# Kernel tuning notes

Hardware: AMD Instinct MI355X
Metric: run time of the kernel (lower is better)

Reference implementation:

```python
import jax, jax.numpy as jnp
import numpy as np

NUM_CLASSES = 3
STRIDES = (8, 16, 32)


def _decode(out, stride):
    # out: [B, 5+C, H, W] -> [B, H*W, 5+C] decoded to image coords; also return grid [H*W, 2]
    B, C, H, W = out.shape
    yv, xv = jnp.meshgrid(jnp.arange(H), jnp.arange(W), indexing='ij')
    grid = jnp.stack([xv, yv], -1).reshape(H * W, 2).astype(out.dtype)
    o = out.reshape(B, C, H * W).transpose(0, 2, 1)
    xy = (o[..., :2] + grid[None]) * stride
    wh = jnp.exp(o[..., 2:4]) * stride
    return jnp.concatenate([xy, wh, o[..., 4:]], -1), grid


def _pairwise_iou(gt, pr):
    # gt [G,4], pr [A,4], cxcywh -> iou [G,A]
    tl = jnp.maximum(gt[:, None, :2] - gt[:, None, 2:] / 2, pr[None, :, :2] - pr[None, :, 2:] / 2)
    br = jnp.minimum(gt[:, None, :2] + gt[:, None, 2:] / 2, pr[None, :, :2] + pr[None, :, 2:] / 2)
    en = (tl < br).all(-1).astype(gt.dtype)
    area_i = jnp.prod(br - tl, -1) * en
    area_u = jnp.prod(gt[:, None, 2:], -1) + jnp.prod(pr[None, :, 2:], -1) - area_i
    return area_i / (area_u + 1e-16)


def _iou_loss(pred, target):
    # elementwise IOUloss (loss_type='iou'): 1 - iou^2, shapes [..., 4]
    tl = jnp.maximum(pred[..., :2] - pred[..., 2:] / 2, target[..., :2] - target[..., 2:] / 2)
    br = jnp.minimum(pred[..., :2] + pred[..., 2:] / 2, target[..., :2] + target[..., 2:] / 2)
    en = (tl < br).all(-1).astype(pred.dtype)
    area_i = jnp.prod(br - tl, -1) * en
    area_u = jnp.prod(pred[..., 2:], -1) + jnp.prod(target[..., 2:], -1) - area_i
    iou = area_i / (area_u + 1e-16)
    return 1.0 - iou ** 2


def _bce_logits(x, y):
    # stable BCEWithLogits, reduction='none'
    return jnp.maximum(x, 0) - x * y + jnp.log1p(jnp.exp(-jnp.abs(x)))


def _assign(gt_boxes, gt_cls, box_p, cls_p, obj_p, xs, ys, strides):
    # SimOTA for one image. gt_boxes [G,4], gt_cls [G], box_p [A,4], cls_p [A,C], obj_p [A,1]
    G = gt_boxes.shape[0]
    C = cls_p.shape[-1]
    xc = (xs + 0.5) * strides  # [A] anchor centers in image coords
    yc = (ys + 0.5) * strides
    # anchors inside gt boxes
    gl = gt_boxes[:, 0:1] - gt_boxes[:, 2:3] / 2
    gr = gt_boxes[:, 0:1] + gt_boxes[:, 2:3] / 2
    gt_ = gt_boxes[:, 1:2] - gt_boxes[:, 3:4] / 2
    gb = gt_boxes[:, 1:2] + gt_boxes[:, 3:4] / 2
    in_box = (xc[None] > gl) & (xc[None] < gr) & (yc[None] > gt_) & (yc[None] < gb)  # [G,A]
    # anchors inside center radius 2.5 * stride
    r = 2.5
    in_ctr = ((xc[None] > gt_boxes[:, 0:1] - r * strides[None]) &
              (xc[None] < gt_boxes[:, 0:1] + r * strides[None]) &
              (yc[None] > gt_boxes[:, 1:2] - r * strides[None]) &
              (yc[None] < gt_boxes[:, 1:2] + r * strides[None]))
    cand = in_box.any(0) | in_ctr.any(0)  # [A] candidate anchors (fg_mask)
    in_both = in_box & in_ctr  # [G,A]
    ious = jnp.where(cand[None], _pairwise_iou(gt_boxes, box_p), 0.0)
    iou_cost = -jnp.log(ious + 1e-8)
    p = jnp.sqrt(jax.nn.sigmoid(cls_p) * jax.nn.sigmoid(obj_p))  # [A,C]
    y = jax.nn.one_hot(gt_cls, C, dtype=p.dtype)  # [G,C]
    cls_cost = -(jnp.einsum('gc,ac->ga', y, jnp.log(p + 1e-8)) +
                 jnp.einsum('gc,ac->ga', 1 - y, jnp.log(1 - p + 1e-8)))
    cost = cls_cost + 3.0 * iou_cost + 1e5 * (~in_both).astype(p.dtype)
    cost = jnp.where(cand[None], cost, 1e9)
    # dynamic-k: k_g = clamp(int(sum of top-10 ious), 1)
    topk_ious, _ = jax.lax.top_k(ious, 10)
    dyn_k = jnp.clip(topk_ious.sum(-1).astype(jnp.int32), 1, None)  # [G]
    ranks = jnp.argsort(jnp.argsort(cost, axis=1), axis=1)
    matching = (ranks < dyn_k[:, None]) & cand[None]  # [G,A]
    # resolve anchors matched to multiple gts by min cost
    multi = matching.sum(0) > 1  # [A]
    best = jnp.arange(G)[:, None] == jnp.argmin(cost, axis=0)[None]  # [G,A]
    matching = jnp.where(multi[None], best, matching)
    fg = matching.any(0)  # [A]
    matched_gt = jnp.argmax(matching, axis=0)  # [A]
    pred_iou = (matching.astype(p.dtype) * ious).sum(0)  # [A]
    cls_t = jax.nn.one_hot(gt_cls[matched_gt], C, dtype=p.dtype) * pred_iou[:, None]  # [A,C]
    reg_t = gt_boxes[matched_gt]  # [A,4]
    return fg, cls_t, reg_t


def _forward(p3, p4, p5, mask_inputs, labels, input_images, mask_labels, now_epoch):
    outs, grids, str_list = [], [], []
    for o, s in zip((p3, p4, p5), STRIDES):
        dec, g = _decode(o, float(s))
        outs.append(dec)
        grids.append(g)
        str_list.append(jnp.full((g.shape[0],), float(s), dtype=dec.dtype))
    outputs = jnp.concatenate(outs, 1)  # [B, A, 5+C]
    xs = jnp.concatenate([g[:, 0] for g in grids], 0)  # [A]
    ys = jnp.concatenate([g[:, 1] for g in grids], 0)
    strides = jnp.concatenate(str_list, 0)
    box_p = outputs[..., :4]
    obj_p = outputs[..., 4:5]
    cls_p = outputs[..., 5:]
    gt_boxes = labels[..., :4]
    gt_cls = labels[..., 4].astype(jnp.int32)
    fg, cls_t, reg_t = jax.vmap(_assign, in_axes=(0, 0, 0, 0, 0, None, None, None))(
        gt_boxes, gt_cls, box_p, cls_p, obj_p, xs, ys, strides)
    # assignment is @torch.no_grad() in the original
    fg, cls_t, reg_t = jax.lax.stop_gradient((fg, cls_t, reg_t))
    fgf = fg.astype(outputs.dtype)  # [B,A]
    num_fg = jnp.maximum(fgf.sum(), 1.0)
    loss_iou = (_iou_loss(box_p, reg_t) * fgf).sum()
    loss_obj = _bce_logits(obj_p[..., 0], fgf).sum()
    loss_cls = (_bce_logits(cls_p, cls_t) * fgf[..., None]).sum()
    # segmentation losses: CE (mean NLL over pixels) + Dice
    logp = jax.nn.log_softmax(mask_inputs, axis=1)  # [B,C,H,W]
    ce = -jnp.take_along_axis(logp, mask_labels[:, None].astype(jnp.int32), axis=1).mean()
    sm = jax.nn.softmax(mask_inputs, axis=1).transpose(0, 2, 3, 1)  # [B,H,W,C]
    oh = jax.nn.one_hot(mask_labels, NUM_CLASSES + 1, dtype=sm.dtype)[..., :NUM_CLASSES]
    tp = (oh * sm).sum((0, 1, 2))
    fp = sm.sum((0, 1, 2)) - tp
    fn = oh.sum((0, 1, 2)) - tp
    smooth = 1e-5
    dice = 1.0 - jnp.mean((2 * tp + smooth) / (2 * tp + fn + fp + smooth))  # beta=1
    loss_mask = ce + dice
    loss_sc = jnp.zeros((), outputs.dtype)  # is_sc=False
    reg_w = 5.0
    total = (reg_w * loss_iou + loss_obj + loss_cls + loss_sc) / num_fg + loss_mask
    return jnp.stack([total, reg_w * loss_iou / num_fg, loss_obj / num_fg,
                      loss_cls / num_fg, loss_mask, loss_sc / num_fg])


def setup_inputs() -> dict:
    key = jax.random.key(0)
    ks = jax.random.split(key, 8)
    B, IMG, G = 8, 1024, 20
    C5 = NUM_CLASSES + 5
    p3 = jax.random.normal(ks[0], (B, C5, 128, 128), jnp.float32)
    p4 = jax.random.normal(ks[1], (B, C5, 64, 64), jnp.float32)
    p5 = jax.random.normal(ks[2], (B, C5, 32, 32), jnp.float32)
    mask_inputs = jax.random.normal(ks[3], (B, NUM_CLASSES, IMG, IMG), jnp.float32)
    cxy = jax.random.uniform(ks[4], (B, G, 2), jnp.float32, 64.0, float(IMG - 64))
    wh = jax.random.uniform(ks[5], (B, G, 2), jnp.float32, 16.0, 256.0)
    cls = jax.random.randint(ks[6], (B, G, 1), 0, NUM_CLASSES).astype(jnp.float32)
    labels = jnp.concatenate([cxy, wh, cls], -1)  # [B,G,5] (cx,cy,w,h,class)
    input_images = jax.random.uniform(ks[7], (B, 1, IMG, IMG), jnp.float32)
    mask_labels = jax.random.randint(jax.random.fold_in(key, 9), (B, IMG, IMG), 0, NUM_CLASSES)
    return {"p3": p3, "p4": p4, "p5": p5, "mask_inputs": mask_inputs,
            "labels": labels, "input_images": input_images,
            "mask_labels": mask_labels, "now_epoch": 0}


def reference(p3, p4, p5, mask_inputs, labels, input_images, mask_labels, now_epoch):
    return _forward(p3, p4, p5, mask_inputs, labels, input_images, mask_labels, now_epoch)
```

## Files before the change

### kernel.cpp

```cpp
#include <hip/hip_runtime.h>
#include <cfloat>

constexpr int A_TOT = 21504;
constexpr int NB    = 8;
constexpr int NG    = 20;
constexpr int HW_M  = 1 << 20;
constexpr int SPLIT = 16;
constexpr int CHUNK = A_TOT / SPLIT;
constexpr int MBLK  = 2048;
constexpr int MS1 = 416, MS2 = 416, MS3 = 800, MS4 = 416;
constexpr int MOFF1 = 0, MOFF2 = 416, MOFF3 = 832, MOFF4 = 1632;

constexpr float L2E = 1.44269504088896340736f;
constexpr float LN2 = 0.69314718055994530942f;

constexpr size_t SZ_GA    = (size_t)NB * NG * A_TOT;
constexpr size_t OFF_IOUS = 0;
constexpr size_t OFF_COST = OFF_IOUS + SZ_GA;
constexpr size_t OFF_THRC = OFF_COST + SZ_GA;
constexpr size_t OFF_THRI = OFF_THRC + NB * NG;
constexpr size_t OFF_PM   = OFF_THRI + NB * NG;
constexpr size_t OFF_PK   = OFF_PM + 672 * 4;
constexpr size_t OFF_PV   = OFF_PK + (size_t)MBLK * 10;
constexpr size_t SZ_PART  = (size_t)NB * NG * SPLIT * 10;
constexpr size_t OFF_PC   = OFF_PV + SZ_PART;
constexpr size_t OFF_PI   = OFF_PC + SZ_PART;

__device__ __forceinline__ float hw_exp2(float x) { return __builtin_amdgcn_exp2f(x); }
__device__ __forceinline__ float hw_log2(float x) { return __builtin_amdgcn_logf(x); }
__device__ __forceinline__ float fexp(float x) { return hw_exp2(x * L2E); }
__device__ __forceinline__ float flog(float x) { return hw_log2(x) * LN2; }
__device__ __forceinline__ float frcp(float x) { return __builtin_amdgcn_rcpf(x); }
__device__ __forceinline__ float fsig(float x) { return frcp(1.f + fexp(-x)); }
__device__ __forceinline__ float fbce(float x, float y) {
  float t = hw_exp2(-fabsf(x) * L2E);
  return fmaxf(x, 0.f) - x * y + LN2 * hw_log2(1.f + t);
}
__device__ __forceinline__ void anchor_geom(int a, int& hw, int& lw, float& st) {
  if (a < 16384)      { hw = a;         lw = 7; st = 8.f;  }
  else if (a < 20480) { hw = a - 16384; lw = 6; st = 16.f; }
  else                { hw = a - 20480; lw = 5; st = 32.f; }
}

__device__ __forceinline__ void merge_desc(float* a, const float* b) {
  float m[16];
  m[0] = a[0]; m[1] = a[1]; m[2] = a[2]; m[3] = a[3]; m[4] = a[4]; m[5] = a[5];
  m[6] = fmaxf(a[6], b[9]); m[7] = fmaxf(a[7], b[8]);
  m[8] = fmaxf(a[8], b[7]); m[9] = fmaxf(a[9], b[6]);
  m[10] = b[5]; m[11] = b[4]; m[12] = b[3]; m[13] = b[2]; m[14] = b[1]; m[15] = b[0];
#pragma unroll
  for (int s = 8; s >= 1; s >>= 1) {
#pragma unroll
    for (int i = 0; i < 16; ++i) {
      if (!(i & s)) {
        float hi = fmaxf(m[i], m[i + s]);
        float lo = fminf(m[i], m[i + s]);
        m[i] = hi; m[i + s] = lo;
      }
    }
  }
#pragma unroll
  for (int j = 0; j < 10; ++j) a[j] = m[j];
}

__device__ __forceinline__ void merge_asc(float* ac, int* ai,
                                          const float* bc, const int* bi) {
  float mc[16]; int mi[16];
#pragma unroll
  for (int i = 0; i < 6; ++i) { mc[i] = ac[i]; mi[i] = ai[i]; }
#pragma unroll
  for (int i = 6; i < 10; ++i) {
    float c2 = bc[15 - i]; int i2 = bi[15 - i];
    bool ta = (ac[i] < c2) || (ac[i] == c2 && ai[i] < i2);
    mc[i] = ta ? ac[i] : c2; mi[i] = ta ? ai[i] : i2;
  }
  mc[10] = bc[5]; mi[10] = bi[5]; mc[11] = bc[4]; mi[11] = bi[4];
  mc[12] = bc[3]; mi[12] = bi[3]; mc[13] = bc[2]; mi[13] = bi[2];
  mc[14] = bc[1]; mi[14] = bi[1]; mc[15] = bc[0]; mi[15] = bi[0];
#pragma unroll
  for (int s = 8; s >= 1; s >>= 1) {
#pragma unroll
    for (int i = 0; i < 16; ++i) {
      if (!(i & s)) {
        float cA = mc[i], cB = mc[i + s];
        int   iA = mi[i], iB = mi[i + s];
        bool ta = (cB < cA) || (cB == cA && iB < iA);
        mc[i]     = ta ? cB : cA; mi[i]     = ta ? iB : iA;
        mc[i + s] = ta ? cA : cB; mi[i + s] = ta ? iA : iB;
      }
    }
  }
#pragma unroll
  for (int j = 0; j < 10; ++j) { ac[j] = mc[j]; ai[j] = mi[j]; }
}

__device__ __forceinline__ void mask_block(int vblk,
    const float* __restrict__ mi, const int* __restrict__ ml,
    float* __restrict__ pk, int tid) {
  int b  = vblk >> 8;
  int g0 = (vblk & 255) << 10;
  const float* base0 = mi + (size_t)b * 3 * HW_M + (size_t)g0 * 4;
  const int*   lbase = ml + ((size_t)b << 20) + (size_t)g0 * 4;

  float4 x0[4], x1[4], x2[4]; int4 lb[4];
#pragma unroll
  for (int u = 0; u < 4; ++u) {
    size_t off = (size_t)(tid + u * 256) * 4;
    x0[u] = *(const float4*)(base0 + off);
    x1[u] = *(const float4*)(base0 + HW_M + off);
    x2[u] = *(const float4*)(base0 + 2 * HW_M + off);
    lb[u] = *(const int4*)(lbase + off);
  }

  float ce = 0.f, tp0 = 0, tp1 = 0, tp2 = 0;
  float ss0 = 0, ss1 = 0, c0 = 0, c1 = 0;

  auto proc = [&](float v0, float v1, float v2, int l) {
    float e0 = hw_exp2(v0 * L2E);
    float e1 = hw_exp2(v1 * L2E);
    float e2 = hw_exp2(v2 * L2E);
    float sum = e0 + e1 + e2;
    float inv = __builtin_amdgcn_rcpf(sum);
    float lse = hw_log2(sum) * LN2;
    float s0 = e0 * inv, s1 = e1 * inv;
    ss0 += s0; ss1 += s1;
    bool l0 = (l == 0), l1 = (l == 1);
    float vl = l0 ? v0 : (l1 ? v1 : v2);
    float el = l0 ? e0 : (l1 ? e1 : e2);
    float sl = el * inv;
    ce += vl - lse;
    tp0 += l0 ? sl : 0.f;
    tp1 += l1 ? sl : 0.f;
    tp2 += (!l0 && !l1) ? sl : 0.f;
    c0 += l0 ? 1.f : 0.f;
    c1 += l1 ? 1.f : 0.f;
  };

#pragma unroll
  for (int u = 0; u < 4; ++u) {
    proc(x0[u].x, x1[u].x, x2[u].x, lb[u].x);
    proc(x0[u].y, x1[u].y, x2[u].y, lb[u].y);
    proc(x0[u].z, x1[u].z, x2[u].z, lb[u].z);
    proc(x0[u].w, x1[u].w, x2[u].w, lb[u].w);
  }
  float ss2 = 16.f - ss0 - ss1;
  float c2 = 16.f - c0 - c1;

  __shared__ float scr[4][10];
  float vals[10] = { ce, tp0, tp1, tp2, ss0, ss1, ss2, c0, c1, c2 };
#pragma unroll
  for (int k = 0; k < 10; ++k) {
    float v = vals[k];
#pragma unroll
    for (int off = 32; off > 0; off >>= 1) v += __shfl_down(v, off, 64);
    if ((tid & 63) == 0) scr[tid >> 6][k] = v;
  }
  __syncthreads();
  if (tid == 0) {
#pragma unroll
    for (int k = 0; k < 10; ++k)
      pk[(size_t)vblk * 10 + k] = scr[0][k] + scr[1][k] + scr[2][k] + scr[3][k];
  }
}

__global__ __launch_bounds__(256) void k_cost_mask(
    const float* __restrict__ p3, const float* __restrict__ p4,
    const float* __restrict__ p5, const float* __restrict__ labels,
    float* __restrict__ ious, float* __restrict__ cost,
    const float* __restrict__ mi, const int* __restrict__ ml,
    float* __restrict__ pk) {
  int bi = blockIdx.x, tid = threadIdx.x;
  if (bi >= 672) { mask_block(MOFF1 + (bi - 672), mi, ml, pk, tid); return; }
  int b = bi / 84, cx = bi - b * 84;

  __shared__ float gt[NG][5];
  if (tid < NG * 5) ((float*)gt)[tid] = labels[b * NG * 5 + tid];
  __syncthreads();
  int a = cx * 256 + tid;

  int hw, lw; float st;
  anchor_geom(a, hw, lw, st);
  const float* src; int HW;
  if (a < 16384)      { src = p3; HW = 16384; }
  else if (a < 20480) { src = p4; HW = 4096;  }
  else                { src = p5; HW = 1024;  }
  int x = hw & ((1 << lw) - 1), y = hw >> lw;
  const float* c0 = src + (size_t)b * 8 * HW + hw;
  float o0 = c0[0];
  float o1 = c0[(size_t)HW];
  float o2 = c0[(size_t)2 * HW];
  float o3 = c0[(size_t)3 * HW];
  float o4 = c0[(size_t)4 * HW];
  float o5 = c0[(size_t)5 * HW];
  float o6 = c0[(size_t)6 * HW];
  float o7 = c0[(size_t)7 * HW];
  float px = (o0 + (float)x) * st, py = (o1 + (float)y) * st;
  float pw = fexp(o2) * st,        ph = fexp(o3) * st;

  float xc = ((float)x + 0.5f) * st, yc = ((float)y + 0.5f) * st;

  float so = fsig(o4);
  float cc0, cc1, cc2, S;
  {
    float q0 = sqrtf(fsig(o5) * so);
    float q1 = sqrtf(fsig(o6) * so);
    float q2 = sqrtf(fsig(o7) * so);
    float lg0 = flog(q0 + 1e-8f), lg1 = flog(q1 + 1e-8f), lg2 = flog(q2 + 1e-8f);
    float m0 = flog(1.f - q0 + 1e-8f), m1 = flog(1.f - q1 + 1e-8f), m2 = flog(1.f - q2 + 1e-8f);
    S = m0 + m1 + m2;
    cc0 = lg0 - m0; cc1 = lg1 - m1; cc2 = lg2 - m2;
  }

  float iouv[NG];
  unsigned bothMask = 0;
  bool anyBox = false, anyCtr = false;
  float hpw = pw * 0.5f, hph = ph * 0.5f;
  float plx = px - hpw, prx = px + hpw, pty = py - hph, pby = py + hph;
  float parea = pw * ph;
  float r = 2.5f * st;

#pragma unroll
  for (int g = 0; g < NG; ++g) {
    float gx = gt[g][0], gy = gt[g][1], gw = gt[g][2], gh = gt[g][3];
    float hgw = gw * 0.5f, hgh = gh * 0.5f;
    float glx = gx - hgw, grx = gx + hgw, gty = gy - hgh, gby = gy + hgh;
    bool ib = (xc > glx) && (xc < grx) && (yc > gty) && (yc < gby);
    bool ic = (xc > gx - r) && (xc < gx + r) && (yc > gy - r) && (yc < gy + r);
    anyBox |= ib; anyCtr |= ic;
    if (ib && ic) bothMask |= (1u << g);
    float tlx = fmaxf(glx, plx), brx = fminf(grx, prx);
    float tly = fmaxf(gty, pty), bry = fminf(gby, pby);
    float en = ((tlx < brx) && (tly < bry)) ? 1.f : 0.f;
    float ai = (brx - tlx) * (bry - tly) * en;
    float au = gw * gh + parea - ai;
    iouv[g] = ai / (au + 1e-16f);
  }
  bool cd = anyBox || anyCtr;

#pragma unroll
  for (int g = 0; g < NG; ++g) {
    float iv = cd ? iouv[g] : 0.f;
    int cg = (int)gt[g][4];
    float ccg = (cg == 0) ? cc0 : ((cg == 1) ? cc1 : cc2);
    float c = -(ccg + S) - 3.f * flog(iv + 1e-8f) +
              (((bothMask >> g) & 1u) ? 0.f : 100000.f);
    size_t idx = ((size_t)(b * NG + g)) * A_TOT + a;
    ious[idx] = iv;
    cost[idx] = cd ? c : 1e9f;
  }
}

__global__ __launch_bounds__(256) void k_topk_mask(
    const float* __restrict__ ious, const float* __restrict__ cost,
    float* __restrict__ pV, float* __restrict__ pC, int* __restrict__ pI,
    const float* __restrict__ mi, const int* __restrict__ ml,
    float* __restrict__ pk) {
  int bi = blockIdx.x, tid = threadIdx.x;
  if (bi >= 640) { mask_block(MOFF2 + (bi - 640), mi, ml, pk, tid); return; }

  int w = tid >> 6, lane = tid & 63;
  int t = bi * 4 + w;
  int b = t / (NG * SPLIT);
  int rem = t - b * (NG * SPLIT);
  int g = rem / SPLIT;
  int s = rem - g * SPLIT;
  int row = b * NG + g;
  int lo = s * CHUNK;
  const float4* iou4 = (const float4*)(ious + (size_t)row * A_TOT + lo);
  const float4* cst4 = (const float4*)(cost + (size_t)row * A_TOT + lo);
  constexpr int NG4 = CHUNK / 4;

  float tv[10];
  float tc[10]; int ti[10];
#pragma unroll
  for (int j = 0; j < 10; ++j) { tv[j] = -1e30f; tc[j] = FLT_MAX; ti[j] = 0x7fffffff; }

  auto insV = [&](float v) {
    if (v > tv[9]) {
#pragma unroll
      for (int j = 0; j < 10; ++j)
        if (v > tv[j]) { float t2 = tv[j]; tv[j] = v; v = t2; }
    }
  };
  auto insC = [&](float c, int ii) {
    if ((c < tc[9]) || (c == tc[9] && ii < ti[9])) {
#pragma unroll
      for (int j = 0; j < 10; ++j) {
        bool lt = (c < tc[j]) || (c == tc[j] && ii < ti[j]);
        if (lt) {
          float t2 = tc[j]; tc[j] = c; c = t2;
          int t3 = ti[j]; ti[j] = ii; ii = t3;
        }
      }
    }
  };

#pragma unroll 1
  for (int grp = lane; grp < NG4; grp += 64) {
    float4 v4 = iou4[grp];
    float4 c4 = cst4[grp];
    int base = lo + grp * 4;
    insV(v4.x); insV(v4.y); insV(v4.z); insV(v4.w);
    insC(c4.x, base); insC(c4.y, base + 1); insC(c4.z, base + 2); insC(c4.w, base + 3);
  }

#pragma unroll 1
  for (int d = 1; d < 64; d <<= 1) {
    float bv[10];
#pragma unroll
    for (int j = 0; j < 10; ++j) bv[j] = __shfl_xor(tv[j], d, 64);
    merge_desc(tv, bv);
  }
#pragma unroll 1
  for (int d = 1; d < 64; d <<= 1) {
    float bc[10]; int bi2[10];
#pragma unroll
    for (int j = 0; j < 10; ++j) {
      bc[j] = __shfl_xor(tc[j], d, 64);
      bi2[j] = __shfl_xor(ti[j], d, 64);
    }
    merge_asc(tc, ti, bc, bi2);
  }

  if (lane == 0) {
    size_t base = ((size_t)row * SPLIT + s) * 10;
#pragma unroll
    for (int j = 0; j < 10; ++j) {
      pV[base + j] = tv[j];
      pC[base + j] = tc[j];
      pI[base + j] = ti[j];
    }
  }
}

__global__ __launch_bounds__(256) void k_merge_mask(
    const float* __restrict__ pV, const float* __restrict__ pC,
    const int* __restrict__ pI, float* __restrict__ thrC, int* __restrict__ thrI,
    const float* __restrict__ mi, const int* __restrict__ ml,
    float* __restrict__ pk) {
  int bi = blockIdx.x, tid = threadIdx.x;
  if (bi >= 160) { mask_block(MOFF3 + (bi - 160), mi, ml, pk, tid); return; }
  int row = bi;
  constexpr int NC = SPLIT * 10;
  __shared__ float sV[NC], sC[NC];
  __shared__ int   sI[NC];
  __shared__ float slot[10];
  __shared__ int kS;

  if (tid < NC) {
    size_t base = (size_t)row * NC + tid;
    sV[tid] = pV[base];
    sC[tid] = pC[base];
    sI[tid] = pI[base];
  }
  __syncthreads();

  float myV = 0.f, myC = 0.f; int myI = 0, rankV = 0;
  if (tid < NC) {
    myV = sV[tid]; myC = sC[tid]; myI = sI[tid];
    for (int j = 0; j < NC; ++j) {
      float v = sV[j];
      rankV += ((v > myV) || (v == myV && j < tid)) ? 1 : 0;
    }
  }
  if (tid < NC && rankV < 10) slot[rankV] = myV;
  __syncthreads();
  if (tid == 0) {
    float sum = 0.f;
#pragma unroll
    for (int j = 0; j < 10; ++j) sum += slot[j];
    int k = (int)sum; if (k < 1) k = 1;
    kS = k;
  }
  __syncthreads();
  if (tid < NC) {
    int rankC = 0;
    for (int j = 0; j < NC; ++j) {
      float c = sC[j];
      rankC += ((c < myC) || (c == myC && sI[j] < myI)) ? 1 : 0;
    }
    if (rankC == kS - 1) { thrC[row] = myC; thrI[row] = myI; }
  }
}

__global__ __launch_bounds__(256) void k_match_mask(
    const float* __restrict__ p3, const float* __restrict__ p4,
    const float* __restrict__ p5, const float* __restrict__ labels,
    const float* __restrict__ cost,
    const float* __restrict__ thrC, const int* __restrict__ thrI,
    float* __restrict__ pm,
    const float* __restrict__ mi, const int* __restrict__ ml,
    float* __restrict__ pk) {
  int bi = blockIdx.x, tid = threadIdx.x;
  if (bi >= 672) { mask_block(MOFF4 + (bi - 672), mi, ml, pk, tid); return; }
  int b = bi / 84, cx = bi - b * 84;

  __shared__ float gt[NG][5];
  __shared__ float tC[NG];
  __shared__ int   tI[NG];
  if (tid < NG * 5) ((float*)gt)[tid] = labels[b * NG * 5 + tid];
  if (tid >= 128 && tid < 128 + NG) tC[tid - 128] = thrC[b * NG + tid - 128];
  if (tid >= 160 && tid < 160 + NG) tI[tid - 160] = thrI[b * NG + tid - 160];
  __syncthreads();
  int a = cx * 256 + tid;

  int hw, lw; float st;
  anchor_geom(a, hw, lw, st);
  const float* src; int HW;
  if (a < 16384)      { src = p3; HW = 16384; }
  else if (a < 20480) { src = p4; HW = 4096;  }
  else                { src = p5; HW = 1024;  }
  int x = hw & ((1 << lw) - 1), y = hw >> lw;
  const float* c0p = src + (size_t)b * 8 * HW + hw;
  float o0 = c0p[0];
  float o1 = c0p[(size_t)HW];
  float o2 = c0p[(size_t)2 * HW];
  float o3 = c0p[(size_t)3 * HW];
  float o4 = c0p[(size_t)4 * HW];
  float o5 = c0p[(size_t)5 * HW];
  float o6 = c0p[(size_t)6 * HW];
  float o7 = c0p[(size_t)7 * HW];
  float px = (o0 + (float)x) * st, py = (o1 + (float)y) * st;
  float pw = fexp(o2) * st,        ph = fexp(o3) * st;

  float xc = ((float)x + 0.5f) * st, yc = ((float)y + 0.5f) * st;

  float iouv[NG];
  bool anyBox = false, anyCtr = false;
  float hpw = pw * 0.5f, hph = ph * 0.5f;
  float plx = px - hpw, prx = px + hpw, pty = py - hph, pby = py + hph;
  float parea = pw * ph;
  float r = 2.5f * st;
#pragma unroll
  for (int g = 0; g < NG; ++g) {
    float gx = gt[g][0], gy = gt[g][1], gw = gt[g][2], gh = gt[g][3];
    float hgw = gw * 0.5f, hgh = gh * 0.5f;
    float glx = gx - hgw, grx = gx + hgw, gty = gy - hgh, gby = gy + hgh;
    bool ib = (xc > glx) && (xc < grx) && (yc > gty) && (yc < gby);
    bool ic = (xc > gx - r) && (xc < gx + r) && (yc > gy - r) && (yc < gy + r);
    anyBox |= ib; anyCtr |= ic;
    float tlx = fmaxf(glx, plx), brx = fminf(grx, prx);
    float tly = fmaxf(gty, pty), bry = fminf(gby, pby);
    float en = ((tlx < brx) && (tly < bry)) ? 1.f : 0.f;
    float ai = (brx - tlx) * (bry - tly) * en;
    float au = gw * gh + parea - ai;
    iouv[g] = ai / (au + 1e-16f);
  }
  bool cd = anyBox || anyCtr;

  int cnt = 0, firstg = -1, gmin = 0;
  float minc = FLT_MAX, pisum = 0.f, iou_gmin = 0.f;
#pragma unroll
  for (int g = 0; g < NG; ++g) {
    size_t idx = ((size_t)(b * NG + g)) * A_TOT + a;
    float c = cost[idx];
    float iv = cd ? iouv[g] : 0.f;
    if (c < minc) { minc = c; gmin = g; iou_gmin = iv; }
    bool m = cd && ((c < tC[g]) || (c == tC[g] && a <= tI[g]));
    if (m) { cnt++; if (firstg < 0) firstg = g; pisum += iv; }
  }
  if (cnt > 1) { firstg = gmin; pisum = iou_gmin; }
  bool fg = cnt > 0;

  float l_obj = fbce(o4, fg ? 1.f : 0.f);
  float l_iou = 0.f, l_cls = 0.f, nfg = fg ? 1.f : 0.f;
  if (fg) {
    float gx = gt[firstg][0], gy = gt[firstg][1];
    float gw = gt[firstg][2], gh = gt[firstg][3];
    int cg = (int)gt[firstg][4];
    float tlx = fmaxf(px - pw * 0.5f, gx - gw * 0.5f);
    float brx = fminf(px + pw * 0.5f, gx + gw * 0.5f);
    float tly = fmaxf(py - ph * 0.5f, gy - gh * 0.5f);
    float bry = fminf(py + ph * 0.5f, gy + gh * 0.5f);
    float en = ((tlx < brx) && (tly < bry)) ? 1.f : 0.f;
    float ai = (brx - tlx) * (bry - tly) * en;
    float au = pw * ph + gw * gh - ai;
    float iou = ai / (au + 1e-16f);
    l_iou = 1.f - iou * iou;
    l_cls  = fbce(o5, (cg == 0) ? pisum : 0.f);
    l_cls += fbce(o6, (cg == 1) ? pisum : 0.f);
    l_cls += fbce(o7, (cg == 2) ? pisum : 0.f);
  }

  __shared__ float scr2[4][4];
  float vals[4] = { nfg, l_iou, l_obj, l_cls };
#pragma unroll
  for (int k = 0; k < 4; ++k) {
    float v = vals[k];
#pragma unroll
    for (int off = 32; off > 0; off >>= 1) v += __shfl_down(v, off, 64);
    if ((tid & 63) == 0) scr2[tid >> 6][k] = v;
  }
  __syncthreads();
  if (tid == 0) {
#pragma unroll
    for (int k = 0; k < 4; ++k)
      pm[(size_t)bi * 4 + k] = scr2[0][k] + scr2[1][k] + scr2[2][k] + scr2[3][k];
  }
}

__device__ __forceinline__ float bsum256(float v, float* scr) {
#pragma unroll
  for (int off = 32; off > 0; off >>= 1) v += __shfl_down(v, off, 64);
  __syncthreads();
  if ((threadIdx.x & 63) == 0) scr[threadIdx.x >> 6] = v;
  __syncthreads();
  return scr[0] + scr[1] + scr[2] + scr[3];
}

__global__ __launch_bounds__(256) void k_final(
    const float* __restrict__ pm, const float* __restrict__ pk,
    float* __restrict__ out) {
  __shared__ float scr[4];
  int tid = threadIdx.x;
  float t0 = 0, t1 = 0, t2 = 0, t3 = 0;
  for (int r = tid; r < 672; r += 256) {
    t0 += pm[(size_t)r * 4 + 0];
    t1 += pm[(size_t)r * 4 + 1];
    t2 += pm[(size_t)r * 4 + 2];
    t3 += pm[(size_t)r * 4 + 3];
  }
  float u[10] = {0,0,0,0,0,0,0,0,0,0};
  for (int r = tid; r < MBLK; r += 256) {
#pragma unroll
    for (int k = 0; k < 10; ++k) u[k] += pk[(size_t)r * 10 + k];
  }
  float S_nfg = bsum256(t0, scr);
  float S_iou = bsum256(t1, scr);
  float S_obj = bsum256(t2, scr);
  float S_cls = bsum256(t3, scr);
  float S_ce  = bsum256(u[0], scr);
  float S_tp0 = bsum256(u[1], scr);
  float S_tp1 = bsum256(u[2], scr);
  float S_tp2 = bsum256(u[3], scr);
  float S_ss0 = bsum256(u[4], scr);
  float S_ss1 = bsum256(u[5], scr);
  float S_ss2 = bsum256(u[6], scr);
  float S_c0  = bsum256(u[7], scr);
  float S_c1  = bsum256(u[8], scr);
  float S_c2  = bsum256(u[9], scr);

  if (tid == 0) {
    float nfg = fmaxf(S_nfg, 1.f);
    float o1 = 5.f * S_iou / nfg;
    float o2 = S_obj / nfg;
    float o3 = S_cls / nfg;
    float ce = -S_ce / (float)((long long)NB << 20);
    float tps[3] = { S_tp0, S_tp1, S_tp2 };
    float sss[3] = { S_ss0, S_ss1, S_ss2 };
    float cns[3] = { S_c0, S_c1, S_c2 };
    float ds = 0.f;
#pragma unroll
    for (int c = 0; c < 3; ++c) {
      float tp = tps[c];
      float fp = sss[c] - tp;
      float fn = cns[c] - tp;
      ds += (2.f * tp + 1e-5f) / (2.f * tp + fn + fp + 1e-5f);
    }
    float dice = 1.f - ds / 3.f;
    float o4 = ce + dice;
    out[0] = o1 + o2 + o3 + o4;
    out[1] = o1;
    out[2] = o2;
    out[3] = o3;
    out[4] = o4;
    out[5] = 0.f;
  }
}

extern "C" void kernel_launch(void* const* d_in, const int* in_sizes, int n_in,
                              void* d_out, int out_size, void* d_ws, size_t ws_size,
                              hipStream_t stream) {
  const float* p3     = (const float*)d_in[0];
  const float* p4     = (const float*)d_in[1];
  const float* p5     = (const float*)d_in[2];
  const float* mi     = (const float*)d_in[3];
  const float* labels = (const float*)d_in[4];
  const int*   ml     = (const int*)d_in[6];

  float* ws   = (float*)d_ws;
  float* ious = ws + OFF_IOUS;
  float* cost = ws + OFF_COST;
  float* thrC = ws + OFF_THRC;
  int*   thrI = (int*)(ws + OFF_THRI);
  float* pm   = ws + OFF_PM;
  float* pk   = ws + OFF_PK;
  float* pV   = ws + OFF_PV;
  float* pC   = ws + OFF_PC;
  int*   pI   = (int*)(ws + OFF_PI);
  float* out  = (float*)d_out;

  k_cost_mask <<<672 + MS1, 256, 0, stream>>>(p3, p4, p5, labels, ious, cost,
                                              mi, ml, pk);
  k_topk_mask <<<640 + MS2, 256, 0, stream>>>(ious, cost, pV, pC, pI,
                                              mi, ml, pk);
  k_merge_mask<<<160 + MS3, 256, 0, stream>>>(pV, pC, pI, thrC, thrI,
                                              mi, ml, pk);
  k_match_mask<<<672 + MS4, 256, 0, stream>>>(p3, p4, p5, labels, cost,
                                              thrC, thrI, pm, mi, ml, pk);
  k_final<<<1, 256, 0, stream>>>(pm, pk, out);
}
```

Measured before the change: 96.80 us.

## Fuse merge and final reduction into preceding kernels via last-block atomics

Removes the separate merge and final-reduction kernels. The last wave to finish each row in the top-k kernel, found with an atomic counter, does the per-row merge using wave shuffles. The last block of the match kernel does the global loss reduction. Mask blocks are redistributed across the three remaining kernels. This cuts launch and inter-kernel drain overhead in exchange for a memset, atomics and a serial tail in the last block.

```diff
diff --git a/kernel.cpp b/kernel.cpp
--- a/kernel.cpp
+++ b/kernel.cpp
@@ -1,5 +1,6 @@
 #include <hip/hip_runtime.h>
 #include <cfloat>
+#include <climits>
 
 constexpr int A_TOT = 21504;
 constexpr int NB    = 8;
@@ -8,8 +9,8 @@
 constexpr int SPLIT = 16;
 constexpr int CHUNK = A_TOT / SPLIT;
 constexpr int MBLK  = 2048;
-constexpr int MS1 = 416, MS2 = 416, MS3 = 800, MS4 = 416;
-constexpr int MOFF1 = 0, MOFF2 = 416, MOFF3 = 832, MOFF4 = 1632;
+constexpr int MS1 = 682, MS2 = 682, MS3 = 684;
+constexpr int MOFF1 = 0, MOFF2 = 682, MOFF3 = 1364;
 
 constexpr float L2E = 1.44269504088896340736f;
 constexpr float LN2 = 0.69314718055994530942f;
@@ -25,6 +26,7 @@
 constexpr size_t SZ_PART  = (size_t)NB * NG * SPLIT * 10;
 constexpr size_t OFF_PC   = OFF_PV + SZ_PART;
 constexpr size_t OFF_PI   = OFF_PC + SZ_PART;
+constexpr size_t OFF_CNT  = OFF_PI + SZ_PART;
 
 __device__ __forceinline__ float hw_exp2(float x) { return __builtin_amdgcn_exp2f(x); }
 __device__ __forceinline__ float hw_log2(float x) { return __builtin_amdgcn_logf(x); }
@@ -253,6 +255,8 @@
 __global__ __launch_bounds__(256) void k_topk_mask(
     const float* __restrict__ ious, const float* __restrict__ cost,
     float* __restrict__ pV, float* __restrict__ pC, int* __restrict__ pI,
+    float* __restrict__ thrC, int* __restrict__ thrI,
+    int* __restrict__ cntRow,
     const float* __restrict__ mi, const int* __restrict__ ml,
     float* __restrict__ pk) {
   int bi = blockIdx.x, tid = threadIdx.x;
@@ -273,7 +277,7 @@
   float tv[10];
   float tc[10]; int ti[10];
 #pragma unroll
-  for (int j = 0; j < 10; ++j) { tv[j] = -1e30f; tc[j] = FLT_MAX; ti[j] = 0x7fffffff; }
+  for (int j = 0; j < 10; ++j) { tv[j] = -1e30f; tc[j] = FLT_MAX; ti[j] = INT_MAX; }
 
   auto insV = [&](float v) {
     if (v > tv[9]) {
@@ -331,240 +335,236 @@
       pI[base + j] = ti[j];
     }
   }
-}
-
-__global__ __launch_bounds__(256) void k_merge_mask(
-    const float* __restrict__ pV, const float* __restrict__ pC,
-    const int* __restrict__ pI, float* __restrict__ thrC, int* __restrict__ thrI,
-    const float* __restrict__ mi, const int* __restrict__ ml,
-    float* __restrict__ pk) {
-  int bi = blockIdx.x, tid = threadIdx.x;
-  if (bi >= 160) { mask_block(MOFF3 + (bi - 160), mi, ml, pk, tid); return; }
-  int row = bi;
-  constexpr int NC = SPLIT * 10;
-  __shared__ float sV[NC], sC[NC];
-  __shared__ int   sI[NC];
-  __shared__ float slot[10];
-  __shared__ int kS;
-
-  if (tid < NC) {
-    size_t base = (size_t)row * NC + tid;
-    sV[tid] = pV[base];
-    sC[tid] = pC[base];
-    sI[tid] = pI[base];
-  }
-  __syncthreads();
-
-  float myV = 0.f, myC = 0.f; int myI = 0, rankV = 0;
-  if (tid < NC) {
-    myV = sV[tid]; myC = sC[tid]; myI = sI[tid];
-    for (int j = 0; j < NC; ++j) {
-      float v = sV[j];
-      rankV += ((v > myV) || (v == myV && j < tid)) ? 1 : 0;
-    }
-  }
-  if (tid < NC && rankV < 10) slot[rankV] = myV;
-  __syncthreads();
-  if (tid == 0) {
-    float sum = 0.f;
-#pragma unroll
-    for (int j = 0; j < 10; ++j) sum += slot[j];
-    int k = (int)sum; if (k < 1) k = 1;
-    kS = k;
-  }
-  __syncthreads();
-  if (tid < NC) {
-    int rankC = 0;
-    for (int j = 0; j < NC; ++j) {
-      float c = sC[j];
-      rankC += ((c < myC) || (c == myC && sI[j] < myI)) ? 1 : 0;
-    }
-    if (rankC == kS - 1) { thrC[row] = myC; thrI[row] = myI; }
-  }
-}
-
-__global__ __launch_bounds__(256) void k_match_mask(
+
+  __threadfence();
+  int old = 0;
+  if (lane == 0) old = atomicAdd(&cntRow[row], 1);
+  old = __shfl(old, 0, 64);
+  if (old == SPLIT - 1) {
+    __threadfence();
+    const float* rowV = pV + (size_t)row * 160;
+    const float* rowC = pC + (size_t)row * 160;
+    const int*   rowI = pI + (size_t)row * 160;
+    float v0 = rowV[lane],      c0v = rowC[lane];      int i0 = rowI[lane];
+    float v1 = rowV[64 + lane], c1v = rowC[64 + lane]; int i1 = rowI[64 + lane];
+    float v2 = -1e30f, c2v = FLT_MAX; int i2 = INT_MAX;
+    if (lane < 32) { v2 = rowV[128 + lane]; c2v = rowC[128 + lane]; i2 = rowI[128 + lane]; }
+    int rv0 = 0, rv1 = 0, rv2 = 0, rc0 = 0, rc1 = 0, rc2 = 0;
+#pragma unroll 1
+    for (int j = 0; j < 160; ++j) {
+      int srcl = j & 63, wreg = j >> 6;
+      float vj = __shfl(wreg == 0 ? v0 : (wreg == 1 ? v1 : v2), srcl, 64);
+      float cj = __shfl(wreg == 0 ? c0v : (wreg == 1 ? c1v : c2v), srcl, 64);
+      int   ij = __shfl(wreg == 0 ? i0 : (wreg == 1 ? i1 : i2), srcl, 64);
+      rv0 += ((vj > v0) || (vj == v0 && j < lane)) ? 1 : 0;
+      rv1 += ((vj > v1) || (vj == v1 && j < 64 + lane)) ? 1 : 0;
+      rv2 += ((vj > v2) || (vj == v2 && j < 128 + lane)) ? 1 : 0;
+      rc0 += ((cj < c0v) || (cj == c0v && ij < i0)) ? 1 : 0;
+      rc1 += ((cj < c1v) || (cj == c1v && ij < i1)) ? 1 : 0;
+      rc2 += ((cj < c2v) || (cj == c2v && ij < i2)) ? 1 : 0;
+    }
+    float s10 = (rv0 < 10 ? v0 : 0.f) + (rv1 < 10 ? v1 : 0.f) +
+                ((lane < 32 && rv2 < 10) ? v2 : 0.f);
+#pragma unroll
+    for (int d = 32; d > 0; d >>= 1) s10 += __shfl_xor(s10, d, 64);
+    int k = (int)s10; if (k < 1) k = 1;
+    if (rc0 == k - 1)              { thrC[row] = c0v; thrI[row] = i0; }
+    if (rc1 == k - 1)              { thrC[row] = c1v; thrI[row] = i1; }
+    if (lane < 32 && rc2 == k - 1) { thrC[row] = c2v; thrI[row] = i2; }
+  }
+}
+
+__global__ __launch_bounds__(256) void k_match_mask_final(
     const float* __restrict__ p3, const float* __restrict__ p4,
     const float* __restrict__ p5, const float* __restrict__ labels,
     const float* __restrict__ cost,
     const float* __restrict__ thrC, const int* __restrict__ thrI,
     float* __restrict__ pm,
     const float* __restrict__ mi, const int* __restrict__ ml,
-    float* __restrict__ pk) {
+    float* __restrict__ pk,
+    int* __restrict__ cntFin, float* __restrict__ out) {
   int bi = blockIdx.x, tid = threadIdx.x;
-  if (bi >= 672) { mask_block(MOFF4 + (bi - 672), mi, ml, pk, tid); return; }
-  int b = bi / 84, cx = bi - b * 84;
-
-  __shared__ float gt[NG][5];
-  __shared__ float tC[NG];
-  __shared__ int   tI[NG];
-  if (tid < NG * 5) ((float*)gt)[tid] = labels[b * NG * 5 + tid];
-  if (tid >= 128 && tid < 128 + NG) tC[tid - 128] = thrC[b * NG + tid - 128];
-  if (tid >= 160 && tid < 160 + NG) tI[tid - 160] = thrI[b * NG + tid - 160];
-  __syncthreads();
-  int a = cx * 256 + tid;
-
-  int hw, lw; float st;
-  anchor_geom(a, hw, lw, st);
-  const float* src; int HW;
-  if (a < 16384)      { src = p3; HW = 16384; }
-  else if (a < 20480) { src = p4; HW = 4096;  }
-  else                { src = p5; HW = 1024;  }
-  int x = hw & ((1 << lw) - 1), y = hw >> lw;
-  const float* c0p = src + (size_t)b * 8 * HW + hw;
-  float o0 = c0p[0];
-  float o1 = c0p[(size_t)HW];
-  float o2 = c0p[(size_t)2 * HW];
-  float o3 = c0p[(size_t)3 * HW];
-  float o4 = c0p[(size_t)4 * HW];
-  float o5 = c0p[(size_t)5 * HW];
-  float o6 = c0p[(size_t)6 * HW];
-  float o7 = c0p[(size_t)7 * HW];
-  float px = (o0 + (float)x) * st, py = (o1 + (float)y) * st;
-  float pw = fexp(o2) * st,        ph = fexp(o3) * st;
-
-  float xc = ((float)x + 0.5f) * st, yc = ((float)y + 0.5f) * st;
-
-  float iouv[NG];
-  bool anyBox = false, anyCtr = false;
-  float hpw = pw * 0.5f, hph = ph * 0.5f;
-  float plx = px - hpw, prx = px + hpw, pty = py - hph, pby = py + hph;
-  float parea = pw * ph;
-  float r = 2.5f * st;
-#pragma unroll
-  for (int g = 0; g < NG; ++g) {
-    float gx = gt[g][0], gy = gt[g][1], gw = gt[g][2], gh = gt[g][3];
-    float hgw = gw * 0.5f, hgh = gh * 0.5f;
-    float glx = gx - hgw, grx = gx + hgw, gty = gy - hgh, gby = gy + hgh;
-    bool ib = (xc > glx) && (xc < grx) && (yc > gty) && (yc < gby);
-    bool ic = (xc > gx - r) && (xc < gx + r) && (yc > gy - r) && (yc < gy + r);
-    anyBox |= ib; anyCtr |= ic;
-    float tlx = fmaxf(glx, plx), brx = fminf(grx, prx);
-    float tly = fmaxf(gty, pty), bry = fminf(gby, pby);
-    float en = ((tlx < brx) && (tly < bry)) ? 1.f : 0.f;
-    float ai = (brx - tlx) * (bry - tly) * en;
-    float au = gw * gh + parea - ai;
-    iouv[g] = ai / (au + 1e-16f);
-  }
-  bool cd = anyBox || anyCtr;
-
-  int cnt = 0, firstg = -1, gmin = 0;
-  float minc = FLT_MAX, pisum = 0.f, iou_gmin = 0.f;
-#pragma unroll
-  for (int g = 0; g < NG; ++g) {
-    size_t idx = ((size_t)(b * NG + g)) * A_TOT + a;
-    float c = cost[idx];
-    float iv = cd ? iouv[g] : 0.f;
-    if (c < minc) { minc = c; gmin = g; iou_gmin = iv; }
-    bool m = cd && ((c < tC[g]) || (c == tC[g] && a <= tI[g]));
-    if (m) { cnt++; if (firstg < 0) firstg = g; pisum += iv; }
-  }
-  if (cnt > 1) { firstg = gmin; pisum = iou_gmin; }
-  bool fg = cnt > 0;
-
-  float l_obj = fbce(o4, fg ? 1.f : 0.f);
-  float l_iou = 0.f, l_cls = 0.f, nfg = fg ? 1.f : 0.f;
-  if (fg) {
-    float gx = gt[firstg][0], gy = gt[firstg][1];
-    float gw = gt[firstg][2], gh = gt[firstg][3];
-    int cg = (int)gt[firstg][4];
-    float tlx = fmaxf(px - pw * 0.5f, gx - gw * 0.5f);
-    float brx = fminf(px + pw * 0.5f, gx + gw * 0.5f);
-    float tly = fmaxf(py - ph * 0.5f, gy - gh * 0.5f);
-    float bry = fminf(py + ph * 0.5f, gy + gh * 0.5f);
-    float en = ((tlx < brx) && (tly < bry)) ? 1.f : 0.f;
-    float ai = (brx - tlx) * (bry - tly) * en;
-    float au = pw * ph + gw * gh - ai;
-    float iou = ai / (au + 1e-16f);
-    l_iou = 1.f - iou * iou;
-    l_cls  = fbce(o5, (cg == 0) ? pisum : 0.f);
-    l_cls += fbce(o6, (cg == 1) ? pisum : 0.f);
-    l_cls += fbce(o7, (cg == 2) ? pisum : 0.f);
-  }
-
-  __shared__ float scr2[4][4];
-  float vals[4] = { nfg, l_iou, l_obj, l_cls };
-#pragma unroll
-  for (int k = 0; k < 4; ++k) {
-    float v = vals[k];
-#pragma unroll
-    for (int off = 32; off > 0; off >>= 1) v += __shfl_down(v, off, 64);
-    if ((tid & 63) == 0) scr2[tid >> 6][k] = v;
-  }
+  if (bi >= 672) {
+    mask_block(MOFF3 + (bi - 672), mi, ml, pk, tid);
+  } else {
+    int b = bi / 84, cx = bi - b * 84;
+
+    __shared__ float gt[NG][5];
+    __shared__ float tC[NG];
+    __shared__ int   tI[NG];
+    if (tid < NG * 5) ((float*)gt)[tid] = labels[b * NG * 5 + tid];
+    if (tid >= 128 && tid < 128 + NG) tC[tid - 128] = thrC[b * NG + tid - 128];
+    if (tid >= 160 && tid < 160 + NG) tI[tid - 160] = thrI[b * NG + tid - 160];
+    __syncthreads();
+    int a = cx * 256 + tid;
+
+    int hw, lw; float st;
+    anchor_geom(a, hw, lw, st);
+    const float* src; int HW;
+    if (a < 16384)      { src = p3; HW = 16384; }
+    else if (a < 20480) { src = p4; HW = 4096;  }
+    else                { src = p5; HW = 1024;  }
+    int x = hw & ((1 << lw) - 1), y = hw >> lw;
+    const float* c0p = src + (size_t)b * 8 * HW + hw;
+    float o0 = c0p[0];
+    float o1 = c0p[(size_t)HW];
+    float o2 = c0p[(size_t)2 * HW];
+    float o3 = c0p[(size_t)3 * HW];
+    float o4 = c0p[(size_t)4 * HW];
+    float o5 = c0p[(size_t)5 * HW];
+    float o6 = c0p[(size_t)6 * HW];
+    float o7 = c0p[(size_t)7 * HW];
+    float px = (o0 + (float)x) * st, py = (o1 + (float)y) * st;
+    float pw = fexp(o2) * st,        ph = fexp(o3) * st;
+
+    float xc = ((float)x + 0.5f) * st, yc = ((float)y + 0.5f) * st;
+
+    float iouv[NG];
+    bool anyBox = false, anyCtr = false;
+    float hpw = pw * 0.5f, hph = ph * 0.5f;
+    float plx = px - hpw, prx = px + hpw, pty = py - hph, pby = py + hph;
+    float parea = pw * ph;
+    float r = 2.5f * st;
+#pragma unroll
+    for (int g = 0; g < NG; ++g) {
+      float gx = gt[g][0], gy = gt[g][1], gw = gt[g][2], gh = gt[g][3];
+      float hgw = gw * 0.5f, hgh = gh * 0.5f;
+      float glx = gx - hgw, grx = gx + hgw, gty = gy - hgh, gby = gy + hgh;
+      bool ib = (xc > glx) && (xc < grx) && (yc > gty) && (yc < gby);
+      bool ic = (xc > gx - r) && (xc < gx + r) && (yc > gy - r) && (yc < gy + r);
+      anyBox |= ib; anyCtr |= ic;
+      float tlx = fmaxf(glx, plx), brx = fminf(grx, prx);
+      float tly = fmaxf(gty, pty), bry = fminf(gby, pby);
+      float en = ((tlx < brx) && (tly < bry)) ? 1.f : 0.f;
+      float ai = (brx - tlx) * (bry - tly) * en;
+      float au = gw * gh + parea - ai;
+      iouv[g] = ai / (au + 1e-16f);
+    }
+    bool cd = anyBox || anyCtr;
+
+    int cnt = 0, firstg = -1, gmin = 0;
+    float minc = FLT_MAX, pisum = 0.f, iou_gmin = 0.f;
+#pragma unroll
+    for (int g = 0; g < NG; ++g) {
+      size_t idx = ((size_t)(b * NG + g)) * A_TOT + a;
+      float c = cost[idx];
+      float iv = cd ? iouv[g] : 0.f;
+      if (c < minc) { minc = c; gmin = g; iou_gmin = iv; }
+      bool m = cd && ((c < tC[g]) || (c == tC[g] && a <= tI[g]));
+      if (m) { cnt++; if (firstg < 0) firstg = g; pisum += iv; }
+    }
+    if (cnt > 1) { firstg = gmin; pisum = iou_gmin; }
+    bool fg = cnt > 0;
+
+    float l_obj = fbce(o4, fg ? 1.f : 0.f);
+    float l_iou = 0.f, l_cls = 0.f, nfg = fg ? 1.f : 0.f;
+    if (fg) {
+      float gx = gt[firstg][0], gy = gt[firstg][1];
+      float gw = gt[firstg][2], gh = gt[firstg][3];
+      int cg = (int)gt[firstg][4];
+      float tlx = fmaxf(px - pw * 0.5f, gx - gw * 0.5f);
+      float brx = fminf(px + pw * 0.5f, gx + gw * 0.5f);
+      float tly = fmaxf(py - ph * 0.5f, gy - gh * 0.5f);
+      float bry = fminf(py + ph * 0.5f, gy + gh * 0.5f);
+      float en = ((tlx < brx) && (tly < bry)) ? 1.f : 0.f;
+      float ai = (brx - tlx) * (bry - tly) * en;
+      float au = pw * ph + gw * gh - ai;
+      float iou = ai / (au + 1e-16f);
+      l_iou = 1.f - iou * iou;
+      l_cls  = fbce(o5, (cg == 0) ? pisum : 0.f);
+      l_cls += fbce(o6, (cg == 1) ? pisum : 0.f);
+      l_cls += fbce(o7, (cg == 2) ? pisum : 0.f);
+    }
+
+    __shared__ float scr2[4][4];
+    float vals[4] = { nfg, l_iou, l_obj, l_cls };
+#pragma unroll
+    for (int k = 0; k < 4; ++k) {
+      float v = vals[k];
+#pragma unroll
+      for (int off = 32; off > 0; off >>= 1) v += __shfl_down(v, off, 64);
+      if ((tid & 63) == 0) scr2[tid >> 6][k] = v;
+    }
+    __syncthreads();
+    if (tid == 0) {
+#pragma unroll
+      for (int k = 0; k < 4; ++k)
+        pm[(size_t)bi * 4 + k] = scr2[0][k] + scr2[1][k] + scr2[2][k] + scr2[3][k];
+    }
+  }
+
+  __shared__ int lastFlag;
   __syncthreads();
   if (tid == 0) {
-#pragma unroll
-    for (int k = 0; k < 4; ++k)
-      pm[(size_t)bi * 4 + k] = scr2[0][k] + scr2[1][k] + scr2[2][k] + scr2[3][k];
-  }
-}
-
-__device__ __forceinline__ float bsum256(float v, float* scr) {
-#pragma unroll
-  for (int off = 32; off > 0; off >>= 1) v += __shfl_down(v, off, 64);
+    __threadfence();
+    int old = atomicAdd(cntFin, 1);
+    lastFlag = (old == (int)gridDim.x - 1) ? 1 : 0;
+  }
   __syncthreads();
-  if ((threadIdx.x & 63) == 0) scr[threadIdx.x >> 6] = v;
-  __syncthreads();
-  return scr[0] + scr[1] + scr[2] + scr[3];
-}
-
-__global__ __launch_bounds__(256) void k_final(
-    const float* __restrict__ pm, const float* __restrict__ pk,
-    float* __restrict__ out) {
-  __shared__ float scr[4];
-  int tid = threadIdx.x;
-  float t0 = 0, t1 = 0, t2 = 0, t3 = 0;
-  for (int r = tid; r < 672; r += 256) {
-    t0 += pm[(size_t)r * 4 + 0];
-    t1 += pm[(size_t)r * 4 + 1];
-    t2 += pm[(size_t)r * 4 + 2];
-    t3 += pm[(size_t)r * 4 + 3];
-  }
-  float u[10] = {0,0,0,0,0,0,0,0,0,0};
-  for (int r = tid; r < MBLK; r += 256) {
-#pragma unroll
-    for (int k = 0; k < 10; ++k) u[k] += pk[(size_t)r * 10 + k];
-  }
-  float S_nfg = bsum256(t0, scr);
-  float S_iou = bsum256(t1, scr);
-  float S_obj = bsum256(t2, scr);
-  float S_cls = bsum256(t3, scr);
-  float S_ce  = bsum256(u[0], scr);
-  float S_tp0 = bsum256(u[1], scr);
-  float S_tp1 = bsum256(u[2], scr);
-  float S_tp2 = bsum256(u[3], scr);
-  float S_ss0 = bsum256(u[4], scr);
-  float S_ss1 = bsum256(u[5], scr);
-  float S_ss2 = bsum256(u[6], scr);
-  float S_c0  = bsum256(u[7], scr);
-  float S_c1  = bsum256(u[8], scr);
-  float S_c2  = bsum256(u[9], scr);
-
-  if (tid == 0) {
-    float nfg = fmaxf(S_nfg, 1.f);
-    float o1 = 5.f * S_iou / nfg;
-    float o2 = S_obj / nfg;
-    float o3 = S_cls / nfg;
-    float ce = -S_ce / (float)((long long)NB << 20);
-    float tps[3] = { S_tp0, S_tp1, S_tp2 };
-    float sss[3] = { S_ss0, S_ss1, S_ss2 };
-    float cns[3] = { S_c0, S_c1, S_c2 };
-    float ds = 0.f;
-#pragma unroll
-    for (int c = 0; c < 3; ++c) {
-      float tp = tps[c];
-      float fp = sss[c] - tp;
-      float fn = cns[c] - tp;
-      ds += (2.f * tp + 1e-5f) / (2.f * tp + fn + fp + 1e-5f);
-    }
-    float dice = 1.f - ds / 3.f;
-    float o4 = ce + dice;
-    out[0] = o1 + o2 + o3 + o4;
-    out[1] = o1;
-    out[2] = o2;
-    out[3] = o3;
-    out[4] = o4;
-    out[5] = 0.f;
+  if (lastFlag) {
+    __threadfence();
+    __shared__ float fscr[4];
+    float t0 = 0, t1 = 0, t2 = 0, t3 = 0;
+    for (int rr = tid; rr < 672; rr += 256) {
+      t0 += pm[(size_t)rr * 4 + 0];
+      t1 += pm[(size_t)rr * 4 + 1];
+      t2 += pm[(size_t)rr * 4 + 2];
+      t3 += pm[(size_t)rr * 4 + 3];
+    }
+    float u[10] = {0,0,0,0,0,0,0,0,0,0};
+    for (int rr = tid; rr < MBLK; rr += 256) {
+#pragma unroll
+      for (int k = 0; k < 10; ++k) u[k] += pk[(size_t)rr * 10 + k];
+    }
+    auto bsum = [&](float v) -> float {
+#pragma unroll
+      for (int off = 32; off > 0; off >>= 1) v += __shfl_down(v, off, 64);
+      __syncthreads();
+      if ((tid & 63) == 0) fscr[tid >> 6] = v;
+      __syncthreads();
+      return fscr[0] + fscr[1] + fscr[2] + fscr[3];
+    };
+    float S_nfg = bsum(t0);
+    float S_iou = bsum(t1);
+    float S_obj = bsum(t2);
+    float S_cls = bsum(t3);
+    float S_ce  = bsum(u[0]);
+    float S_tp0 = bsum(u[1]);
+    float S_tp1 = bsum(u[2]);
+    float S_tp2 = bsum(u[3]);
+    float S_ss0 = bsum(u[4]);
+    float S_ss1 = bsum(u[5]);
+    float S_ss2 = bsum(u[6]);
+    float S_c0  = bsum(u[7]);
+    float S_c1  = bsum(u[8]);
+    float S_c2  = bsum(u[9]);
+
+    if (tid == 0) {
+      float nfg = fmaxf(S_nfg, 1.f);
+      float o1 = 5.f * S_iou / nfg;
+      float o2 = S_obj / nfg;
+      float o3 = S_cls / nfg;
+      float ce = -S_ce / (float)((long long)NB << 20);
+      float tps[3] = { S_tp0, S_tp1, S_tp2 };
+      float sss[3] = { S_ss0, S_ss1, S_ss2 };
+      float cns[3] = { S_c0, S_c1, S_c2 };
+      float ds = 0.f;
+#pragma unroll
+      for (int c = 0; c < 3; ++c) {
+        float tp = tps[c];
+        float fp = sss[c] - tp;
+        float fn = cns[c] - tp;
+        ds += (2.f * tp + 1e-5f) / (2.f * tp + fn + fp + 1e-5f);
+      }
+      float dice = 1.f - ds / 3.f;
+      float o4v = ce + dice;
+      out[0] = o1 + o2 + o3 + o4v;
+      out[1] = o1;
+      out[2] = o2;
+      out[3] = o3;
+      out[4] = o4v;
+      out[5] = 0.f;
+    }
   }
 }
 
@@ -588,15 +588,17 @@
   float* pV   = ws + OFF_PV;
   float* pC   = ws + OFF_PC;
   int*   pI   = (int*)(ws + OFF_PI);
+  int*   cntRow = (int*)(ws + OFF_CNT);
+  int*   cntFin = cntRow + 160;
   float* out  = (float*)d_out;
 
-  k_cost_mask <<<672 + MS1, 256, 0, stream>>>(p3, p4, p5, labels, ious, cost,
-                                              mi, ml, pk);
-  k_topk_mask <<<640 + MS2, 256, 0, stream>>>(ious, cost, pV, pC, pI,
-                                              mi, ml, pk);
-  k_merge_mask<<<160 + MS3, 256, 0, stream>>>(pV, pC, pI, thrC, thrI,
-                                              mi, ml, pk);
-  k_match_mask<<<672 + MS4, 256, 0, stream>>>(p3, p4, p5, labels, cost,
-                                              thrC, thrI, pm, mi, ml, pk);
-  k_final<<<1, 256, 0, stream>>>(pm, pk, out);
-}
+  hipMemsetAsync(cntRow, 0, 161 * sizeof(int), stream);
+
+  k_cost_mask<<<672 + MS1, 256, 0, stream>>>(p3, p4, p5, labels, ious, cost,
+                                             mi, ml, pk);
+  k_topk_mask<<<640 + MS2, 256, 0, stream>>>(ious, cost, pV, pC, pI,
+                                             thrC, thrI, cntRow, mi, ml, pk);
+  k_match_mask_final<<<672 + MS3, 256, 0, stream>>>(p3, p4, p5, labels, cost,
+                                                    thrC, thrI, pm, mi, ml, pk,
+                                                    cntFin, out);
+}
```

After: 233.5 us. +141.2%, slower.
